# Kernel optimization log

Measured on AMD Instinct MI355X. Metric: run time of the kernel, lower is better.

## Reference

```python
import jax, jax.numpy as jnp
import numpy as np

B, H, W = 64, 224, 224
EPS = 1e-5


def setup_inputs() -> dict:
    key = jax.random.key(0)
    ks = jax.random.split(key, 8)
    n = lambda k, s, std: jax.random.normal(k, s, jnp.float32) * std
    return {
        "x": jax.random.normal(ks[0], (B, 1, H, W), jnp.float32),
        "conv1_w": n(ks[1], (24, 1, 3, 3), 0.2),
        "conv1_b": jnp.zeros((24,), jnp.float32),
        "bn1_g": jnp.ones((24,), jnp.float32),
        "bn1_b": jnp.zeros((24,), jnp.float32),
        "conv2_w": n(ks[2], (48, 24, 3, 3), 0.07),
        "conv2_b": jnp.zeros((48,), jnp.float32),
        "bn2_g": jnp.ones((48,), jnp.float32),
        "bn2_b": jnp.zeros((48,), jnp.float32),
        "fconv_w": n(ks[3], (48, 48, 56, 56), 0.003),
        "fconv_b": jnp.zeros((48,), jnp.float32),
        "lin1_w": n(ks[4], (24, 48), 0.02),
        "lin1_b": jnp.zeros((24,), jnp.float32),
        "lin2_w": n(ks[5], (4, 24), 0.01),
        "lin2_b": jnp.array([0.0, 0.0, 1.0, 0.0], jnp.float32),  # torch init: identity transform bias
    }


def conv2d(x, w, b):
    y = jax.lax.conv_general_dilated(x, w, (1, 1), ((1, 1), (1, 1)),
                                     dimension_numbers=("NCHW", "OIHW", "NCHW"))
    return y + b[None, :, None, None]


def batchnorm(x, g, b):
    # train-mode BN: batch statistics over (N, H, W), biased variance
    m = x.mean((0, 2, 3), keepdims=True)
    v = x.var((0, 2, 3), keepdims=True)
    return (x - m) * jax.lax.rsqrt(v + EPS) * g[None, :, None, None] + b[None, :, None, None]


def maxpool2(x):
    b, c, h, w = x.shape
    return x.reshape(b, c, h // 2, 2, w // 2, 2).max(axis=(3, 5))


def affine_grid(theta, h, w):
    # theta: [B,2,3]; align_corners=False normalized coords (torch default)
    xs = (jnp.arange(w, dtype=jnp.float32) * 2 + 1) / w - 1.0
    ys = (jnp.arange(h, dtype=jnp.float32) * 2 + 1) / h - 1.0
    gx, gy = jnp.meshgrid(xs, ys)                      # [H,W] each
    base = jnp.stack([gx, gy, jnp.ones_like(gx)], -1)  # [H,W,3] (x, y, 1)
    return jnp.einsum("bij,hwj->bhwi", theta, base)    # [B,H,W,2] -> (x, y)


def grid_sample(img, grid):
    # bilinear, zeros padding, align_corners=False (torch defaults)
    b, c, h, w = img.shape
    ix = ((grid[..., 0] + 1.0) * w - 1.0) * 0.5        # [B,H,W]
    iy = ((grid[..., 1] + 1.0) * h - 1.0) * 0.5
    x0 = jnp.floor(ix); y0 = jnp.floor(iy)
    x1 = x0 + 1.0; y1 = y0 + 1.0
    wx1 = ix - x0; wx0 = 1.0 - wx1
    wy1 = iy - y0; wy0 = 1.0 - wy1
    bidx = jnp.arange(b)[:, None, None]

    def tap(xf, yf, wgt):
        valid = (xf >= 0) & (xf < w) & (yf >= 0) & (yf < h)
        xi = jnp.clip(xf, 0, w - 1).astype(jnp.int32)
        yi = jnp.clip(yf, 0, h - 1).astype(jnp.int32)
        vals = img[bidx, :, yi, xi]                    # [B,H,W,C]
        return vals * (wgt * valid)[..., None]

    out = (tap(x0, y0, wx0 * wy0) + tap(x1, y0, wx1 * wy0)
           + tap(x0, y1, wx0 * wy1) + tap(x1, y1, wx1 * wy1))
    return jnp.transpose(out, (0, 3, 1, 2))            # [B,C,H,W]


def reference(x, conv1_w, conv1_b, bn1_g, bn1_b, conv2_w, conv2_b, bn2_g, bn2_b,
              fconv_w, fconv_b, lin1_w, lin1_b, lin2_w, lin2_b):
    b, _, h, w = x.shape
    x1 = maxpool2(jax.nn.relu(batchnorm(conv2d(x, conv1_w, conv1_b), bn1_g, bn1_b)))
    x1 = maxpool2(jax.nn.relu(batchnorm(conv2d(x1, conv2_w, conv2_b), bn2_g, bn2_b)))
    # final_conv with kernel 56 over a 56x56 map == full contraction
    feat = jnp.einsum("bchw,ochw->bo", x1, fconv_w) + fconv_b      # [B,48]
    theta4 = jax.nn.relu(feat @ lin1_w.T + lin1_b) @ lin2_w.T + lin2_b  # [B,4]
    tx, ty, scale, angle = theta4[:, 0], theta4[:, 1], theta4[:, 2], theta4[:, 3]
    c, s = jnp.cos(angle), jnp.sin(angle)
    # (T @ R @ S)[:, :2] built directly, fully vectorized over batch
    row0 = jnp.stack([scale * c, -scale * s, tx], -1)
    row1 = jnp.stack([scale * s, scale * c, ty], -1)
    theta = jnp.stack([row0, row1], 1)                 # [B,2,3]
    grid = affine_grid(theta, h, w)
    out = grid_sample(x, grid)
    return out, tx, ty, scale, angle
```

## Files before the change

### kernel.cpp

```cpp
#include <hip/hip_runtime.h>
#include <hip/hip_bf16.h>

#define NB 64
#define H0 224
#define W0 224
#define C1 24
#define C2 48
#define H1 112
#define W1 112
#define H2 56
#define W2 56
#define EPSV 1e-5f

#define WS_STATS1   0
#define WS_STATS2   432
#define WS_FEAT     1296
#define WS_B2       4368
#define WS_X2       11280
#define WS_FWT      (WS_X2 + 4818944)
#define WS_X1       9645072
#define WS_NEED_BIG ((size_t)(WS_X1 + 9633792) * 4)
#define OUT0_ELEMS  (NB*H0*W0)

typedef _Float16 v8h __attribute__((ext_vector_type(8)));
typedef float    v4f __attribute__((ext_vector_type(4)));

static __device__ __forceinline__ unsigned short f2h(float v) {
    _Float16 h = (_Float16)v;
    unsigned short us;
    __builtin_memcpy(&us, &h, 2);
    return us;
}

__global__ __launch_bounds__(256) void k_zero1(float* __restrict__ ws)
{
    int t = blockIdx.x * 256 + threadIdx.x;
    if (t < 432) ws[t] = 0.f;
}

__global__ __launch_bounds__(256) void k_stats_prep(
    const float* __restrict__ x, const float* __restrict__ w1, const float* __restrict__ b1,
    const float* __restrict__ w2, const float* __restrict__ fw,
    float* __restrict__ ws, _Float16* __restrict__ x1g, _Float16* __restrict__ fwt)
{
    __shared__ __align__(16) unsigned char smem[18432];
    const int tid = threadIdx.x;
    const int bid = blockIdx.x;

    if (bid >= 3136) {
        _Float16 (*T)[136] = (_Float16(*)[136])smem;
        const int p = bid - 3136;
        if (p < 54) {
            int t = p * 256 + tid;
            if (t >= 432 && t < WS_B2) ws[t] = 0.f;
            if (t < 13824) {
                int e = t & 7;
                int l = (t >> 3) & 63;
                int g = t >> 9;
                int q = l >> 4, ml = l & 15;
                int kp = g / 3, nt = g % 3;
                int ic = q * 8 + e;
                int oc = nt * 16 + ml;
                float v = (ic < C1) ? w2[(oc * C1 + ic) * 9 + kp] : 0.f;
                ((_Float16*)(ws + WS_B2))[t] = (_Float16)v;
            }
        }
        const int kb = p * 128;
#pragma unroll
        for (int t3 = 0; t3 < 6; t3++) {
            int li = tid + 256 * t3;
            int o = li >> 5, k4 = li & 31;
            float4 v = *(const float4*)&fw[(long)o * 150528 + kb + 4 * k4];
            T[o][4 * k4 + 0] = (_Float16)v.x;
            T[o][4 * k4 + 1] = (_Float16)v.y;
            T[o][4 * k4 + 2] = (_Float16)v.z;
            T[o][4 * k4 + 3] = (_Float16)v.w;
        }
        __syncthreads();
        uint4* dst = (uint4*)&fwt[(long)kb * 48];
#pragma unroll
        for (int t3 = 0; t3 < 3; t3++) {
            int u = tid + 256 * t3;
            int gg = u / 384;
            int rem = u % 384;
            int o = rem >> 3;
            int k8 = (rem & 7) * 8;
            dst[u] = *(const uint4*)&T[o][gg * 64 + k8];
        }
        return;
    }

    float (*xt)[36] = (float(*)[36])smem;
    unsigned int (*outt)[13] = (unsigned int(*)[13])(smem + 4896);
    float* sred = (float*)(smem + 18208);

    const int b = bid / 49;
    const int rem0 = bid % 49;
    const int py0 = (rem0 / 7) * 16, px0 = (rem0 % 7) * 16;
    const int iy0 = 2 * py0 - 1, ix0 = 2 * px0 - 1;
    const float* xb = x + b * (H0 * W0);

    for (int li = tid; li < 34 * 34; li += 256) {
        int ry = li / 34, rx = li % 34;
        int gy = iy0 + ry, gx = ix0 + rx;
        bool ok = (gy >= 0) & (gy < H0) & (gx >= 0) & (gx < W0);
        xt[ry][rx] = ok ? xb[gy * W0 + gx] : 0.f;
    }

    const int wid = tid >> 6;
    const int lane = tid & 63;
    const int c0 = wid * 6;

    const int c0s = __builtin_amdgcn_readfirstlane(c0);
    const float* __restrict__ wps = w1 + c0s * 9;
    float wr[54], br[6];
#pragma unroll
    for (int k = 0; k < 54; k++) wr[k] = wps[k];
#pragma unroll
    for (int c = 0; c < 6; c++) br[c] = b1[c0s + c];

    __syncthreads();

    float s[6] = {0.f, 0.f, 0.f, 0.f, 0.f, 0.f};
    float q[6] = {0.f, 0.f, 0.f, 0.f, 0.f, 0.f};
    const int pc = lane & 15;
    const int pr0 = lane >> 4;

#pragma unroll
    for (int pp = 0; pp < 4; pp++) {
        const int pr = pr0 + 4 * pp;
        float patch[16];
#pragma unroll
        for (int i2 = 0; i2 < 4; i2++)
#pragma unroll
            for (int j2 = 0; j2 < 4; j2++)
                patch[i2 * 4 + j2] = xt[2 * pr + i2][2 * pc + j2];

        unsigned int pk[3];
#pragma unroll
        for (int cp = 0; cp < 3; cp++) {
            unsigned int pv = 0;
#pragma unroll
            for (int h = 0; h < 2; h++) {
                int c = 2 * cp + h;
                float m4 = -1e30f;
#pragma unroll
                for (int sy = 0; sy < 2; sy++)
#pragma unroll
                    for (int sx = 0; sx < 2; sx++) {
                        float a = br[c];
#pragma unroll
                        for (int ky = 0; ky < 3; ky++)
#pragma unroll
                            for (int kx = 0; kx < 3; kx++)
                                a = fmaf(patch[(sy + ky) * 4 + (sx + kx)], wr[c * 9 + ky * 3 + kx], a);
                        s[c] += a;
                        q[c] = fmaf(a, a, q[c]);
                        m4 = fmaxf(m4, a);
                    }
                pv |= ((unsigned int)f2h(m4)) << (16 * h);
            }
            pk[cp] = pv;
        }
        int pos = pr * 16 + pc;
        outt[pos][wid * 3 + 0] = pk[0];
        outt[pos][wid * 3 + 1] = pk[1];
        outt[pos][wid * 3 + 2] = pk[2];
    }

#pragma unroll
    for (int c = 0; c < 6; c++) {
#pragma unroll
        for (int off = 32; off > 0; off >>= 1) {
            s[c] += __shfl_down(s[c], off, 64);
            q[c] += __shfl_down(q[c], off, 64);
        }
    }
    if (lane == 0) {
#pragma unroll
        for (int c = 0; c < 6; c++) {
            sred[c0 + c] = s[c];
            sred[C1 + c0 + c] = q[c];
        }
    }
    __syncthreads();

    if (tid < 2 * C1) {
        atomicAdd(&ws[WS_STATS1 + (bid & 7) * 2 * C1 + tid], sred[tid]);
    }

    for (int u = tid; u < 768; u += 256) {
        int pos = u / 3, prt = u % 3;
        int pr = pos >> 4, pcc = pos & 15;
        long p = (long)(b * H1 + (py0 + pr)) * W1 + (px0 + pcc);
        uint4 v;
        v.x = outt[pos][4 * prt + 0];
        v.y = outt[pos][4 * prt + 1];
        v.z = outt[pos][4 * prt + 2];
        v.w = outt[pos][4 * prt + 3];
        *(uint4*)(x1g + p * C1 + prt * 8) = v;
    }
}

__global__ __launch_bounds__(256, 2) void k_conv2_fused5(
    const _Float16* __restrict__ x1g, const _Float16* __restrict__ bpp,
    const float* __restrict__ g1, const float* __restrict__ bb1,
    const float* __restrict__ b2,
    float* __restrict__ ws, unsigned int* __restrict__ pooltu)
{
    __shared__ __align__(16) _Float16 x1t[2][10][18][32];
    __shared__ float alds[C1], bflds[C1];
    __shared__ float sred[2 * C2];

    const int tid = threadIdx.x;
    const int w = tid >> 6;
    const int lane = tid & 63;
    const int ml = lane & 15;
    const int qq = lane >> 4;

    v8h B[9][3];
#pragma unroll
    for (int kp = 0; kp < 9; kp++)
#pragma unroll
        for (int nt = 0; nt < 3; nt++)
            B[kp][nt] = *(const v8h*)&bpp[((kp * 3 + nt) * 64 + lane) * 8];

    if (tid < C1) {
        float s = 0.f, q = 0.f;
#pragma unroll
        for (int i = 0; i < 8; i++) {
            s += ws[WS_STATS1 + i * 2 * C1 + tid];
            q += ws[WS_STATS1 + i * 2 * C1 + C1 + tid];
        }
        const float N = (float)(NB * H0 * W0);
        float m = s / N;
        float v = q / N - m * m;
        float a = g1[tid] / sqrtf(v + EPSV);
        alds[tid] = a;
        bflds[tid] = bb1[tid] - m * a;
    }
    if (tid < 2 * C2) sred[tid] = 0.f;

    float bias[3] = {b2[ml], b2[16 + ml], b2[32 + ml]};

    int spart[3], spr[3], spc[3]; bool swrite[3];
#pragma unroll
    for (int it3 = 0; it3 < 3; it3++) {
        int li = tid + it3 * 256;
        swrite[it3] = li < 720;
        spart[it3] = li & 3;
        int pos = li >> 2;
        spr[it3] = pos / 18;
        spc[it3] = pos % 18;
    }

    const int nb = gridDim.x;
    const int NTILE = 6272;
    int qn = NTILE / nb, rn = NTILE % nb;
    int start = (blockIdx.x < rn) ? blockIdx.x * (qn + 1)
                                  : rn * (qn + 1) + (blockIdx.x - rn) * qn;
    int cnt = (blockIdx.x < rn) ? qn + 1 : qn;

    float svacc[3] = {0.f, 0.f, 0.f}, qvacc[3] = {0.f, 0.f, 0.f};

    v8h raw[3];
    bool inb_n[3];
    {
        int t = start;
        int tb = t / 98, rem = t % 98;
        int ty = (rem / 7) * 8, txx = (rem % 7) * 16;
#pragma unroll
        for (int it3 = 0; it3 < 3; it3++) {
#pragma unroll
            for (int e = 0; e < 8; e++) raw[it3][e] = (_Float16)0.f;
            int gy = ty - 1 + spr[it3], gx = txx - 1 + spc[it3];
            inb_n[it3] = swrite[it3] & (spart[it3] < 3) &
                         (gy >= 0) & (gy < H1) & (gx >= 0) & (gx < W1);
            if (inb_n[it3])
                raw[it3] = *(const v8h*)&x1g[((tb * H1 + gy) * W1 + gx) * C1 + spart[it3] * 8];
        }
    }
    __syncthreads();

#pragma unroll
    for (int it3 = 0; it3 < 3; it3++) {
        if (swrite[it3]) {
            v8h r8;
            if (inb_n[it3]) {
#pragma unroll
                for (int e = 0; e < 8; e++) {
                    int c = spart[it3] * 8 + e;
                    float vv = fmaxf(fmaf((float)raw[it3][e], alds[c], bflds[c]), 0.f);
                    r8[e] = (_Float16)vv;
                }
            } else {
#pragma unroll
                for (int e = 0; e < 8; e++) r8[e] = (_Float16)0.f;
            }
            *(v8h*)&x1t[0][spr[it3]][spc[it3]][spart[it3] * 8] = r8;
        }
    }
    __syncthreads();

    for (int it = 0; it < cnt; it++) {
        const int cur = it & 1;
        const int t = start + it;
        const int tb = t / 98, rem = t % 98;
        const int ty = (rem / 7) * 8, txx = (rem % 7) * 16;

        const bool haveNext = (it + 1 < cnt);
        if (haveNext) {
            int t2 = t + 1;
            int nb2 = t2 / 98, rem2 = t2 % 98;
            int ny = (rem2 / 7) * 8, nx = (rem2 % 7) * 16;
#pragma unroll
            for (int it3 = 0; it3 < 3; it3++) {
#pragma unroll
                for (int e = 0; e < 8; e++) raw[it3][e] = (_Float16)0.f;
                int gy = ny - 1 + spr[it3], gx = nx - 1 + spc[it3];
                inb_n[it3] = swrite[it3] & (spart[it3] < 3) &
                             (gy >= 0) & (gy < H1) & (gx >= 0) & (gx < W1);
                if (inb_n[it3])
                    raw[it3] = *(const v8h*)&x1g[((nb2 * H1 + gy) * W1 + gx) * C1 + spart[it3] * 8];
            }
        }

        v4f acc[2][3];
#pragma unroll
        for (int mt = 0; mt < 2; mt++)
#pragma unroll
            for (int nt = 0; nt < 3; nt++)
                acc[mt][nt] = (v4f){0.f, 0.f, 0.f, 0.f};

#pragma unroll
        for (int kp = 0; kp < 9; kp++) {
            const int ky = kp / 3, kx = kp % 3;
#pragma unroll
            for (int mt = 0; mt < 2; mt++) {
                const int r = 2 * w + mt;
                v8h a = *(const v8h*)&x1t[cur][r + ky][ml + kx][qq * 8];
                acc[mt][0] = __builtin_amdgcn_mfma_f32_16x16x32_f16(a, B[kp][0], acc[mt][0], 0, 0, 0);
                acc[mt][1] = __builtin_amdgcn_mfma_f32_16x16x32_f16(a, B[kp][1], acc[mt][1], 0, 0, 0);
                acc[mt][2] = __builtin_amdgcn_mfma_f32_16x16x32_f16(a, B[kp][2], acc[mt][2], 0, 0, 0);
            }
        }

#pragma unroll
        for (int nt = 0; nt < 3; nt++) {
            int oc = nt * 16 + ml;
            float z[2][4];
#pragma unroll
            for (int mt = 0; mt < 2; mt++)
#pragma unroll
                for (int rg = 0; rg < 4; rg++) {
                    float val = acc[mt][nt][rg] + bias[nt];
                    z[mt][rg] = val;
                    svacc[nt] += val;
                    qvacc[nt] = fmaf(val, val, qvacc[nt]);
                }
            int py = (ty >> 1) + w;
            float m0 = fmaxf(fmaxf(z[0][0], z[0][1]), fmaxf(z[1][0], z[1][1]));
            float m1 = fmaxf(fmaxf(z[0][2], z[0][3]), fmaxf(z[1][2], z[1][3]));
            int px0 = (txx >> 1) + qq * 2;
            int k = oc * 3136 + py * W2 + px0;
            unsigned int pk2 = (unsigned int)f2h(m0) | ((unsigned int)f2h(m1) << 16);
            pooltu[(((k >> 6) * NB + tb) << 5) + ((k & 63) >> 1)] = pk2;
        }

        if (haveNext) {
#pragma unroll
            for (int it3 = 0; it3 < 3; it3++) {
                if (swrite[it3]) {
                    v8h r8;
                    if (inb_n[it3]) {
#pragma unroll
                        for (int e = 0; e < 8; e++) {
                            int c = spart[it3] * 8 + e;
                            float vv = fmaxf(fmaf((float)raw[it3][e], alds[c], bflds[c]), 0.f);
                            r8[e] = (_Float16)vv;
                        }
                    } else {
#pragma unroll
                        for (int e = 0; e < 8; e++) r8[e] = (_Float16)0.f;
                    }
                    *(v8h*)&x1t[cur ^ 1][spr[it3]][spc[it3]][spart[it3] * 8] = r8;
                }
            }
        }
        __syncthreads();
    }

#pragma unroll
    for (int nt = 0; nt < 3; nt++) {
        float sv = svacc[nt], qv = qvacc[nt];
        sv += __shfl_xor(sv, 16, 64); qv += __shfl_xor(qv, 16, 64);
        sv += __shfl_xor(sv, 32, 64); qv += __shfl_xor(qv, 32, 64);
        if (qq == 0) {
            atomicAdd(&sred[nt * 16 + ml], sv);
            atomicAdd(&sred[C2 + nt * 16 + ml], qv);
        }
    }
    __syncthreads();
    if (tid < 2 * C2) {
        atomicAdd(&ws[WS_STATS2 + (blockIdx.x & 7) * 2 * C2 + tid], sred[tid]);
    }
}

__global__ __launch_bounds__(256) void k_fconv6(
    const unsigned int* __restrict__ pooltu, const _Float16* __restrict__ fwt,
    const float* __restrict__ ws, const float* __restrict__ g2, const float* __restrict__ bb2,
    float* __restrict__ feat)
{
    __shared__ __align__(16) _Float16 fwh[48][136];
    __shared__ __align__(16) _Float16 x2h[64][136];
    __shared__ float csh[2 * C2];

    const int tid = threadIdx.x;
    const int bx = blockIdx.x;

    const uint4* fsrc = (const uint4*)fwt + (long)bx * 768;
    const uint4* psrc = (const uint4*)pooltu + (long)bx * 1024;
    uint4 fr[3], pr[4];
#pragma unroll
    for (int t3 = 0; t3 < 3; t3++) fr[t3] = fsrc[tid + 256 * t3];
#pragma unroll
    for (int t4 = 0; t4 < 4; t4++) pr[t4] = psrc[tid + 256 * t4];

    if (tid < C2) {
        int c = tid;
        float s = 0.f, q = 0.f;
#pragma unroll
        for (int i = 0; i < 8; i++) {
            s += ws[WS_STATS2 + i * 2 * C2 + c];
            q += ws[WS_STATS2 + i * 2 * C2 + C2 + c];
        }
        const float N = (float)(NB * H1 * W1);
        float m = s / N;
        float v = q / N - m * m;
        float a = g2[c] / sqrtf(v + EPSV);
        csh[c] = a;
        csh[C2 + c] = bb2[c] - m * a;
    }
    __syncthreads();

#pragma unroll
    for (int t3 = 0; t3 < 3; t3++) {
        int li = tid + 256 * t3;
        int gg = li / 384;
        int o = (li % 384) / 8;
        int kin = (li & 7) * 8;
        *(uint4*)&fwh[o][gg * 64 + kin] = fr[t3];
    }
    const int c0 = (2 * bx) / 49, c1 = (2 * bx + 1) / 49;
    const float a0 = csh[c0], bf0 = csh[C2 + c0];
    const float a1 = csh[c1], bf1 = csh[C2 + c1];
#pragma unroll
    for (int t4 = 0; t4 < 4; t4++) {
        int li = tid + 256 * t4;
        int gg = li >> 9;
        int b = (li & 511) >> 3;
        int kin = (li & 7) * 8;
        float aa = gg ? a1 : a0;
        float bb = gg ? bf1 : bf0;
        union { uint4 u; v8h h; } cv;
        cv.u = pr[t4];
        v8h r8;
#pragma unroll
        for (int e = 0; e < 8; e++)
            r8[e] = (_Float16)fmaxf(fmaf((float)cv.h[e], aa, bb), 0.f);
        *(v8h*)&x2h[b][gg * 64 + kin] = r8;
    }
    __syncthreads();

    const int w = tid >> 6;
    const int lane = tid & 63;
    const int ml = lane & 15;
    const int qq = lane >> 4;

    v4f acc[3];
#pragma unroll
    for (int ot = 0; ot < 3; ot++) acc[ot] = (v4f){0.f, 0.f, 0.f, 0.f};

#pragma unroll
    for (int ks = 0; ks < 4; ks++) {
        v8h a = *(const v8h*)&x2h[w * 16 + ml][ks * 32 + qq * 8];
#pragma unroll
        for (int ot = 0; ot < 3; ot++) {
            v8h bb = *(const v8h*)&fwh[ot * 16 + ml][ks * 32 + qq * 8];
            acc[ot] = __builtin_amdgcn_mfma_f32_16x16x32_f16(a, bb, acc[ot], 0, 0, 0);
        }
    }

#pragma unroll
    for (int ot = 0; ot < 3; ot++)
#pragma unroll
        for (int rg = 0; rg < 4; rg++)
            atomicAdd(&feat[(w * 16 + qq * 4 + rg) * C2 + ot * 16 + ml], acc[ot][rg]);
}

__global__ __launch_bounds__(256) void k_sample4(
    const float* __restrict__ x, const float* __restrict__ feat, const float* __restrict__ fcb,
    const float* __restrict__ l1w, const float* __restrict__ l1b,
    const float* __restrict__ l2w, const float* __restrict__ l2b,
    float* __restrict__ out)
{
    __shared__ float hsh[24];
    __shared__ float th[4];
    const int b = blockIdx.y;
    const int tid = threadIdx.x;
    if (tid < 24) {
        float a = l1b[tid];
#pragma unroll
        for (int o = 0; o < C2; o++)
            a = fmaf(feat[b * C2 + o] + fcb[o], l1w[tid * C2 + o], a);
        hsh[tid] = fmaxf(a, 0.f);
    }
    __syncthreads();
    if (tid < 4) {
        float a = l2b[tid];
#pragma unroll
        for (int jj = 0; jj < 24; jj++) a = fmaf(hsh[jj], l2w[tid * 24 + jj], a);
        th[tid] = a;
        if (blockIdx.x == 0) out[OUT0_ELEMS + tid * NB + b] = a;
    }
    __syncthreads();

    const float tx = th[0], ty = th[1], sc = th[2], an = th[3];
    const float cc = cosf(an), ss = sinf(an);
    const float t00 = sc * cc, t01 = -sc * ss, t10 = sc * ss, t11 = sc * cc;
    const float* xb = x + b * (H0 * W0);

    int idx = (blockIdx.x * 256 + tid) * 2;
    int i = idx / W0, j = idx % W0;
    float ys = (2.f * (float)i + 1.f) / (float)H0 - 1.f;

    float o2[2];
#pragma unroll
    for (int px = 0; px < 2; px++) {
        float xs = (2.f * (float)(j + px) + 1.f) / (float)W0 - 1.f;
        float gx = t00 * xs + t01 * ys + tx;
        float gy = t10 * xs + t11 * ys + ty;
        float ix = ((gx + 1.f) * (float)W0 - 1.f) * 0.5f;
        float iy = ((gy + 1.f) * (float)H0 - 1.f) * 0.5f;
        float x0 = floorf(ix), y0 = floorf(iy);
        float x1f = x0 + 1.f, y1f = y0 + 1.f;
        float wx1 = ix - x0, wx0 = 1.f - wx1;
        float wy1 = iy - y0, wy0 = 1.f - wy1;
        auto tap = [&](float xf, float yf, float wgt) -> float {
            bool valid = (xf >= 0.f) & (xf < (float)W0) & (yf >= 0.f) & (yf < (float)H0);
            int xi = (int)fminf(fmaxf(xf, 0.f), (float)(W0 - 1));
            int yi = (int)fminf(fmaxf(yf, 0.f), (float)(H0 - 1));
            return valid ? xb[yi * W0 + xi] * wgt : 0.f;
        };
        o2[px] = tap(x0, y0, wx0 * wy0) + tap(x1f, y0, wx1 * wy0)
               + tap(x0, y1f, wx0 * wy1) + tap(x1f, y1f, wx1 * wy1);
    }
    *(float2*)&out[(b * H0 + i) * W0 + j] = make_float2(o2[0], o2[1]);
}

__global__ __launch_bounds__(256) void k_init(const float* __restrict__ w2, float* __restrict__ ws)
{
    int t = blockIdx.x * 256 + threadIdx.x;
    if (t < WS_B2) ws[t] = 0.f;
    if (t < 13824) {
        int e = t & 7;
        int l = (t >> 3) & 63;
        int g = t >> 9;
        int q = l >> 4, ml = l & 15;
        int kp = g / 3, nt = g % 3;
        int ic = q * 8 + e;
        int oc = nt * 16 + ml;
        float v = (ic < C1) ? w2[(oc * C1 + ic) * 9 + kp] : 0.f;
        ((_Float16*)(ws + WS_B2))[t] = (_Float16)v;
    }
}

__global__ __launch_bounds__(256) void k_conv1_stats(
    const float* __restrict__ x, const float* __restrict__ w1, const float* __restrict__ b1,
    float* __restrict__ ws)
{
    float s[C1], q[C1];
#pragma unroll
    for (int c = 0; c < C1; c++) { s[c] = 0.f; q[c] = 0.f; }
    const int NT = gridDim.x * 256;
    const int total = NB * H0 * W0;
    for (int p = blockIdx.x * 256 + threadIdx.x; p < total; p += NT) {
        int b = p / (H0 * W0);
        int r = p % (H0 * W0);
        int y = r / W0;
        int xx = r % W0;
        const float* xb = x + b * (H0 * W0);
        float patch[9];
#pragma unroll
        for (int dy = 0; dy < 3; dy++)
#pragma unroll
            for (int dx = 0; dx < 3; dx++) {
                int yy = y + dy - 1, xc = xx + dx - 1;
                bool ok = (yy >= 0) & (yy < H0) & (xc >= 0) & (xc < W0);
                patch[dy * 3 + dx] = ok ? xb[yy * W0 + xc] : 0.f;
            }
#pragma unroll
        for (int c = 0; c < C1; c++) {
            const float* wp = w1 + c * 9;
            float a = b1[c];
#pragma unroll
            for (int k = 0; k < 9; k++) a = fmaf(patch[k], wp[k], a);
            s[c] += a;
            q[c] = fmaf(a, a, q[c]);
        }
    }
#pragma unroll
    for (int c = 0; c < C1; c++) {
#pragma unroll
        for (int off = 32; off > 0; off >>= 1) {
            s[c] += __shfl_down(s[c], off, 64);
            q[c] += __shfl_down(q[c], off, 64);
        }
    }
    __shared__ float sred[2 * C1];
    if (threadIdx.x < 2 * C1) sred[threadIdx.x] = 0.f;
    __syncthreads();
    if ((threadIdx.x & 63) == 0) {
#pragma unroll
        for (int c = 0; c < C1; c++) {
            atomicAdd(&sred[c], s[c]);
            atomicAdd(&sred[C1 + c], q[c]);
        }
    }
    __syncthreads();
    if (threadIdx.x < 2 * C1) {
        atomicAdd(&ws[WS_STATS1 + (blockIdx.x & 7) * 2 * C1 + threadIdx.x], sred[threadIdx.x]);
    }
}

__global__ __launch_bounds__(256, 2) void k_conv2_fused(
    const float* __restrict__ x, const float* __restrict__ w1, const float* __restrict__ b1,
    const float* __restrict__ g1, const float* __restrict__ bb1,
    const _Float16* __restrict__ bpp, const float* __restrict__ b2,
    float* __restrict__ ws, float* __restrict__ pool)
{
    __shared__ float xt[22][38];
    __shared__ __align__(16) _Float16 x1t[10][18][32];
    __shared__ __align__(16) _Float16 Blds[13824];
    __shared__ float wlds[C1 * 9];
    __shared__ float blds[C1], alds[C1], bflds[C1];
    __shared__ float sred[2 * C2];

    const int tid = threadIdx.x;
    const int b = blockIdx.z;
    const int y0 = blockIdx.y * 8;
    const int x0 = blockIdx.x * 16;
    const float* xb = x + b * (H0 * W0);

    for (int li = tid; li < 13824 / 8; li += 256)
        ((uint4*)Blds)[li] = ((const uint4*)bpp)[li];

    if (tid < C1 * 9) wlds[tid] = w1[tid];
    if (tid < C1) {
        float s = 0.f, q = 0.f;
#pragma unroll
        for (int i = 0; i < 8; i++) {
            s += ws[WS_STATS1 + i * 2 * C1 + tid];
            q += ws[WS_STATS1 + i * 2 * C1 + C1 + tid];
        }
        const float N = (float)(NB * H0 * W0);
        float m = s / N;
        float v = q / N - m * m;
        float a = g1[tid] / sqrtf(v + EPSV);
        blds[tid] = b1[tid];
        alds[tid] = a;
        bflds[tid] = bb1[tid] - m * a;
    }
    if (tid < 2 * C2) sred[tid] = 0.f;

    const int oy0 = 2 * y0 - 3, ox0 = 2 * x0 - 3;
    for (int li = tid; li < 22 * 38; li += 256) {
        int ry = li / 38, rx = li % 38;
        int gy = oy0 + ry, gx = ox0 + rx;
        bool ok = (gy >= 0) & (gy < H0) & (gx >= 0) & (gx < W0);
        xt[ry][rx] = ok ? xb[gy * W0 + gx] : 0.f;
    }
    __syncthreads();

    if (tid < 180) {
        int pr = tid / 18, pc = tid % 18;
        int gy = y0 - 1 + pr, gx = x0 - 1 + pc;
        bool valid = (gy >= 0) & (gy < H1) & (gx >= 0) & (gx < W1);
        float patch[16];
#pragma unroll
        for (int dy = 0; dy < 4; dy++)
#pragma unroll
            for (int dx = 0; dx < 4; dx++)
                patch[dy * 4 + dx] = xt[2 * pr + dy][2 * pc + dx];
        unsigned int* dst = (unsigned int*)&x1t[pr][pc][0];
#pragma unroll
        for (int cp = 0; cp < 12; cp++) {
            unsigned int pk = 0;
#pragma unroll
            for (int h = 0; h < 2; h++) {
                int c = 2 * cp + h;
                float m4 = -1e30f;
#pragma unroll
                for (int py = 0; py < 2; py++)
#pragma unroll
                    for (int px = 0; px < 2; px++) {
                        float a = blds[c];
#pragma unroll
                        for (int ky = 0; ky < 3; ky++)
#pragma unroll
                            for (int kx = 0; kx < 3; kx++)
                                a = fmaf(patch[(py + ky) * 4 + (px + kx)], wlds[c * 9 + ky * 3 + kx], a);
                        m4 = fmaxf(m4, fmaf(a, alds[c], bflds[c]));
                    }
                float v = valid ? fmaxf(m4, 0.f) : 0.f;
                pk |= ((unsigned int)f2h(v)) << (16 * h);
            }
            dst[cp] = pk;
        }
        dst[12] = 0; dst[13] = 0; dst[14] = 0; dst[15] = 0;
    }
    __syncthreads();

    const int w = tid >> 6;
    const int lane = tid & 63;
    const int ml = lane & 15;
    const int q = lane >> 4;

    v4f acc[2][3];
#pragma unroll
    for (int mt = 0; mt < 2; mt++)
#pragma unroll
        for (int nt = 0; nt < 3; nt++)
            acc[mt][nt] = (v4f){0.f, 0.f, 0.f, 0.f};

#pragma unroll
    for (int kp = 0; kp < 9; kp++) {
        const int ky = kp / 3, kx = kp % 3;
        v8h B0 = *(const v8h*)&Blds[((kp * 3 + 0) * 64 + lane) * 8];
        v8h B1 = *(const v8h*)&Blds[((kp * 3 + 1) * 64 + lane) * 8];
        v8h B2 = *(const v8h*)&Blds[((kp * 3 + 2) * 64 + lane) * 8];
#pragma unroll
        for (int mt = 0; mt < 2; mt++) {
            const int r = 2 * w + mt;
            v8h a = *(const v8h*)&x1t[r + ky][ml + kx][q * 8];
            acc[mt][0] = __builtin_amdgcn_mfma_f32_16x16x32_f16(a, B0, acc[mt][0], 0, 0, 0);
            acc[mt][1] = __builtin_amdgcn_mfma_f32_16x16x32_f16(a, B1, acc[mt][1], 0, 0, 0);
            acc[mt][2] = __builtin_amdgcn_mfma_f32_16x16x32_f16(a, B2, acc[mt][2], 0, 0, 0);
        }
    }

#pragma unroll
    for (int nt = 0; nt < 3; nt++) {
        int oc = nt * 16 + ml;
        float bias = b2[oc];
        float z[2][4];
        float sv = 0.f, qv = 0.f;
#pragma unroll
        for (int mt = 0; mt < 2; mt++)
#pragma unroll
            for (int rg = 0; rg < 4; rg++) {
                float val = acc[mt][nt][rg] + bias;
                z[mt][rg] = val;
                sv += val;
                qv = fmaf(val, val, qv);
            }
        sv += __shfl_xor(sv, 16, 64); qv += __shfl_xor(qv, 16, 64);
        sv += __shfl_xor(sv, 32, 64); qv += __shfl_xor(qv, 32, 64);
        if (q == 0) { atomicAdd(&sred[oc], sv); atomicAdd(&sred[C2 + oc], qv); }

        int py = (y0 >> 1) + w;
#pragma unroll
        for (int j = 0; j < 2; j++) {
            float m = fmaxf(fmaxf(z[0][2 * j], z[0][2 * j + 1]),
                            fmaxf(z[1][2 * j], z[1][2 * j + 1]));
            int px = (x0 >> 1) + q * 2 + j;
            pool[((b * C2 + oc) * H2 + py) * W2 + px] = m;
        }
    }
    __syncthreads();
    if (tid < 2 * C2) {
        int cp = (blockIdx.x + 7 * blockIdx.y + 31 * blockIdx.z) & 7;
        atomicAdd(&ws[WS_STATS2 + cp * 2 * C2 + tid], sred[tid]);
    }
}

#define KC 512
#define KSUB 128
__global__ __launch_bounds__(256) void k_fconv(
    const float* __restrict__ pool, const float* __restrict__ ws,
    const float* __restrict__ g2, const float* __restrict__ bb2,
    const float* __restrict__ fw, float* __restrict__ feat)
{
    __shared__ float fwt[C2][KSUB + 1];
    __shared__ float x2t[NB][KSUB + 1];
    __shared__ float csh[2 * C2];
    if (threadIdx.x < C2) {
        int c = threadIdx.x;
        float s = 0.f, q = 0.f;
#pragma unroll
        for (int i = 0; i < 8; i++) {
            s += ws[WS_STATS2 + i * 2 * C2 + c];
            q += ws[WS_STATS2 + i * 2 * C2 + C2 + c];
        }
        const float N = (float)(NB * H1 * W1);
        float m = s / N;
        float v = q / N - m * m;
        float a = g2[c] / sqrtf(v + EPSV);
        csh[c] = a;
        csh[C2 + c] = bb2[c] - m * a;
    }
    int k0 = blockIdx.x * KC;
    int i = threadIdx.x / 16, j = threadIdx.x % 16;
    float acc[3][4] = {{0.f}};
    for (int sub = 0; sub < KC / KSUB; sub++) {
        int kb = k0 + sub * KSUB;
        __syncthreads();
        for (int li = threadIdx.x; li < C2 * KSUB; li += 256) {
            int o = li / KSUB, k = li % KSUB;
            fwt[o][k] = fw[o * 150528 + kb + k];
        }
        for (int li = threadIdx.x; li < NB * KSUB; li += 256) {
            int b = li / KSUB, k = li % KSUB;
            int kk = kb + k;
            int c = kk / (H2 * W2);
            float v = pool[b * 150528 + kk];
            x2t[b][k] = fmaxf(fmaf(v, csh[c], csh[C2 + c]), 0.f);
        }
        __syncthreads();
        for (int k = 0; k < KSUB; k++) {
            float fa[3], xv[4];
#pragma unroll
            for (int c = 0; c < 3; c++) fa[c] = fwt[i + 16 * c][k];
#pragma unroll
            for (int d = 0; d < 4; d++) xv[d] = x2t[j + 16 * d][k];
#pragma unroll
            for (int c = 0; c < 3; c++)
#pragma unroll
                for (int d = 0; d < 4; d++)
                    acc[c][d] = fmaf(fa[c], xv[d], acc[c][d]);
        }
    }
#pragma unroll
    for (int c = 0; c < 3; c++)
#pragma unroll
        for (int d = 0; d < 4; d++)
            atomicAdd(&feat[(j + 16 * d) * C2 + (i + 16 * c)], acc[c][d]);
}

__global__ __launch_bounds__(256) void k_sample(
    const float* __restrict__ x, const float* __restrict__ feat, const float* __restrict__ fcb,
    const float* __restrict__ l1w, const float* __restrict__ l1b,
    const float* __restrict__ l2w, const float* __restrict__ l2b,
    float* __restrict__ out)
{
    __shared__ float hsh[24];
    __shared__ float th[4];
    int b = blockIdx.y;
    int tid = threadIdx.x;
    if (tid < 24) {
        float a = l1b[tid];
        for (int o = 0; o < C2; o++)
            a = fmaf(feat[b * C2 + o] + fcb[o], l1w[tid * C2 + o], a);
        hsh[tid] = fmaxf(a, 0.f);
    }
    __syncthreads();
    if (tid < 4) {
        float a = l2b[tid];
        for (int jj = 0; jj < 24; jj++) a = fmaf(hsh[jj], l2w[tid * 24 + jj], a);
        th[tid] = a;
        if (blockIdx.x == 0) out[OUT0_ELEMS + tid * NB + b] = a;
    }
    __syncthreads();

    int idx = blockIdx.x * 256 + tid;
    int i = idx / W0, j = idx % W0;
    float tx = th[0], ty = th[1], sc = th[2], an = th[3];
    float cc = cosf(an), ss = sinf(an);
    float t00 = sc * cc, t01 = -sc * ss, t10 = sc * ss, t11 = sc * cc;
    float xs = (2.f * (float)j + 1.f) / (float)W0 - 1.f;
    float ys = (2.f * (float)i + 1.f) / (float)H0 - 1.f;
    float gx = t00 * xs + t01 * ys + tx;
    float gy = t10 * xs + t11 * ys + ty;
    float ix = ((gx + 1.f) * (float)W0 - 1.f) * 0.5f;
    float iy = ((gy + 1.f) * (float)H0 - 1.f) * 0.5f;
    float x0 = floorf(ix), y0 = floorf(iy);
    float x1f = x0 + 1.f, y1f = y0 + 1.f;
    float wx1 = ix - x0, wx0 = 1.f - wx1;
    float wy1 = iy - y0, wy0 = 1.f - wy1;
    const float* xb = x + b * (H0 * W0);
    auto tap = [&](float xf, float yf, float wgt) -> float {
        bool valid = (xf >= 0.f) & (xf < (float)W0) & (yf >= 0.f) & (yf < (float)H0);
        int xi = (int)fminf(fmaxf(xf, 0.f), (float)(W0 - 1));
        int yi = (int)fminf(fmaxf(yf, 0.f), (float)(H0 - 1));
        return valid ? xb[yi * W0 + xi] * wgt : 0.f;
    };
    float o = tap(x0, y0, wx0 * wy0) + tap(x1f, y0, wx1 * wy0)
            + tap(x0, y1f, wx0 * wy1) + tap(x1f, y1f, wx1 * wy1);
    out[(b * H0 + i) * W0 + j] = o;
}

extern "C" void kernel_launch(void* const* d_in, const int* in_sizes, int n_in,
                              void* d_out, int out_size, void* d_ws, size_t ws_size,
                              hipStream_t stream)
{
    const float* x    = (const float*)d_in[0];
    const float* c1w  = (const float*)d_in[1];
    const float* c1b  = (const float*)d_in[2];
    const float* bn1g = (const float*)d_in[3];
    const float* bn1b = (const float*)d_in[4];
    const float* c2w  = (const float*)d_in[5];
    const float* c2b  = (const float*)d_in[6];
    const float* bn2g = (const float*)d_in[7];
    const float* bn2b = (const float*)d_in[8];
    const float* fw   = (const float*)d_in[9];
    const float* fcb  = (const float*)d_in[10];
    const float* l1w  = (const float*)d_in[11];
    const float* l1b  = (const float*)d_in[12];
    const float* l2w  = (const float*)d_in[13];
    const float* l2b  = (const float*)d_in[14];
    float* ws  = (float*)d_ws;
    float* out = (float*)d_out;

    if (ws_size >= WS_NEED_BIG) {
        k_zero1<<<dim3(2), 256, 0, stream>>>(ws);
        k_stats_prep<<<dim3(4312), 256, 0, stream>>>(
            x, c1w, c1b, c2w, fw, ws, (_Float16*)(ws + WS_X1), (_Float16*)(ws + WS_FWT));
        k_conv2_fused5<<<dim3(512), 256, 0, stream>>>(
            (const _Float16*)(ws + WS_X1), (const _Float16*)(ws + WS_B2),
            bn1g, bn1b, c2b, ws, (unsigned int*)(ws + WS_X2));
        k_fconv6<<<dim3(1176), 256, 0, stream>>>(
            (const unsigned int*)(ws + WS_X2), (const _Float16*)(ws + WS_FWT),
            ws, bn2g, bn2b, ws + WS_FEAT);
        k_sample4<<<dim3(98, 64), 256, 0, stream>>>(
            x, ws + WS_FEAT, fcb, l1w, l1b, l2w, l2b, out);
    } else {
        k_init<<<dim3(54), 256, 0, stream>>>(c2w, ws);
        k_conv1_stats<<<dim3(1024), 256, 0, stream>>>(x, c1w, c1b, ws);
        k_conv2_fused<<<dim3(7, 14, 64), 256, 0, stream>>>(
            x, c1w, c1b, bn1g, bn1b, (const _Float16*)(ws + WS_B2), c2b, ws, ws + WS_X2);
        k_fconv<<<dim3(150528 / KC), 256, 0, stream>>>(ws + WS_X2, ws, bn2g, bn2b, fw, ws + WS_FEAT);
        k_sample<<<dim3(196, 64), 256, 0, stream>>>(x, ws + WS_FEAT, fcb, l1w, l1b, l2w, l2b, out);
    }
}
```

Measured before the change: 220.0 us.

## Enlarge conv2 spatial tile to 16x16 with 4 M-tiles per wave

The conv2 fused kernel now processes 16x16 output tiles instead of 8x16, so each wave computes four row M-tiles and writes two pooled rows per tile. This halves the tile count and shrinks the relative halo overhead on the shared-memory staging loads. Staging now fills only the 24 real channels with a 3-way split, and the padding slots are zeroed once up front. The cost is doubled LDS and more accumulator registers, which may lower occupancy under the 2-blocks-per-SM launch bound. The tiny zeroing kernel is also replaced by hipMemsetAsync.

```diff
diff --git a/kernel.cpp b/kernel.cpp
--- a/kernel.cpp
+++ b/kernel.cpp
@@ -30,12 +30,6 @@
     unsigned short us;
     __builtin_memcpy(&us, &h, 2);
     return us;
-}
-
-__global__ __launch_bounds__(256) void k_zero1(float* __restrict__ ws)
-{
-    int t = blockIdx.x * 256 + threadIdx.x;
-    if (t < 432) ws[t] = 0.f;
 }
 
 __global__ __launch_bounds__(256) void k_stats_prep(
@@ -202,13 +196,13 @@
     }
 }
 
-__global__ __launch_bounds__(256, 2) void k_conv2_fused5(
+__global__ __launch_bounds__(256, 2) void k_conv2_fused6(
     const _Float16* __restrict__ x1g, const _Float16* __restrict__ bpp,
     const float* __restrict__ g1, const float* __restrict__ bb1,
     const float* __restrict__ b2,
     float* __restrict__ ws, unsigned int* __restrict__ pooltu)
 {
-    __shared__ __align__(16) _Float16 x1t[2][10][18][32];
+    __shared__ __align__(16) _Float16 x1t[2][18][18][32];
     __shared__ float alds[C1], bflds[C1];
     __shared__ float sred[2 * C2];
 
@@ -241,21 +235,32 @@
     }
     if (tid < 2 * C2) sred[tid] = 0.f;
 
+    {
+        v8h z8;
+#pragma unroll
+        for (int e = 0; e < 8; e++) z8[e] = (_Float16)0.f;
+        for (int li = tid; li < 2 * 18 * 18; li += 256) {
+            int bu = li / 324, pos = li % 324;
+            *(v8h*)&x1t[bu][pos / 18][pos % 18][24] = z8;
+        }
+    }
+
     float bias[3] = {b2[ml], b2[16 + ml], b2[32 + ml]};
 
-    int spart[3], spr[3], spc[3]; bool swrite[3];
-#pragma unroll
-    for (int it3 = 0; it3 < 3; it3++) {
-        int li = tid + it3 * 256;
-        swrite[it3] = li < 720;
-        spart[it3] = li & 3;
-        int pos = li >> 2;
-        spr[it3] = pos / 18;
-        spc[it3] = pos % 18;
+    int spart[4], spr[4], spc[4]; bool sv[4];
+#pragma unroll
+    for (int s4 = 0; s4 < 4; s4++) {
+        int li = tid + s4 * 256;
+        sv[s4] = li < 972;
+        int part = li % 3;
+        int pos = li / 3;
+        spart[s4] = part;
+        spr[s4] = pos / 18;
+        spc[s4] = pos % 18;
     }
 
     const int nb = gridDim.x;
-    const int NTILE = 6272;
+    const int NTILE = 3136;
     int qn = NTILE / nb, rn = NTILE % nb;
     int start = (blockIdx.x < rn) ? blockIdx.x * (qn + 1)
                                   : rn * (qn + 1) + (blockIdx.x - rn) * qn;
@@ -263,41 +268,40 @@
 
     float svacc[3] = {0.f, 0.f, 0.f}, qvacc[3] = {0.f, 0.f, 0.f};
 
-    v8h raw[3];
-    bool inb_n[3];
+    v8h raw[4];
+    bool inb_n[4];
     {
         int t = start;
-        int tb = t / 98, rem = t % 98;
-        int ty = (rem / 7) * 8, txx = (rem % 7) * 16;
-#pragma unroll
-        for (int it3 = 0; it3 < 3; it3++) {
-#pragma unroll
-            for (int e = 0; e < 8; e++) raw[it3][e] = (_Float16)0.f;
-            int gy = ty - 1 + spr[it3], gx = txx - 1 + spc[it3];
-            inb_n[it3] = swrite[it3] & (spart[it3] < 3) &
-                         (gy >= 0) & (gy < H1) & (gx >= 0) & (gx < W1);
-            if (inb_n[it3])
-                raw[it3] = *(const v8h*)&x1g[((tb * H1 + gy) * W1 + gx) * C1 + spart[it3] * 8];
-        }
-    }
-    __syncthreads();
-
-#pragma unroll
-    for (int it3 = 0; it3 < 3; it3++) {
-        if (swrite[it3]) {
+        int tb = t / 49, rem = t % 49;
+        int ty = (rem / 7) * 16, txx = (rem % 7) * 16;
+#pragma unroll
+        for (int s4 = 0; s4 < 4; s4++) {
+#pragma unroll
+            for (int e = 0; e < 8; e++) raw[s4][e] = (_Float16)0.f;
+            int gy = ty - 1 + spr[s4], gx = txx - 1 + spc[s4];
+            inb_n[s4] = sv[s4] & (gy >= 0) & (gy < H1) & (gx >= 0) & (gx < W1);
+            if (inb_n[s4])
+                raw[s4] = *(const v8h*)&x1g[((tb * H1 + gy) * W1 + gx) * C1 + spart[s4] * 8];
+        }
+    }
+    __syncthreads();
+
+#pragma unroll
+    for (int s4 = 0; s4 < 4; s4++) {
+        if (sv[s4]) {
             v8h r8;
-            if (inb_n[it3]) {
+            if (inb_n[s4]) {
 #pragma unroll
                 for (int e = 0; e < 8; e++) {
-                    int c = spart[it3] * 8 + e;
-                    float vv = fmaxf(fmaf((float)raw[it3][e], alds[c], bflds[c]), 0.f);
+                    int c = spart[s4] * 8 + e;
+                    float vv = fmaxf(fmaf((float)raw[s4][e], alds[c], bflds[c]), 0.f);
                     r8[e] = (_Float16)vv;
                 }
             } else {
 #pragma unroll
                 for (int e = 0; e < 8; e++) r8[e] = (_Float16)0.f;
             }
-            *(v8h*)&x1t[0][spr[it3]][spc[it3]][spart[it3] * 8] = r8;
+            *(v8h*)&x1t[0][spr[s4]][spc[s4]][spart[s4] * 8] = r8;
         }
     }
     __syncthreads();
@@ -305,29 +309,28 @@
     for (int it = 0; it < cnt; it++) {
         const int cur = it & 1;
         const int t = start + it;
-        const int tb = t / 98, rem = t % 98;
-        const int ty = (rem / 7) * 8, txx = (rem % 7) * 16;
+        const int tb = t / 49, rem = t % 49;
+        const int ty = (rem / 7) * 16, txx = (rem % 7) * 16;
 
         const bool haveNext = (it + 1 < cnt);
         if (haveNext) {
             int t2 = t + 1;
-            int nb2 = t2 / 98, rem2 = t2 % 98;
-            int ny = (rem2 / 7) * 8, nx = (rem2 % 7) * 16;
-#pragma unroll
-            for (int it3 = 0; it3 < 3; it3++) {
-#pragma unroll
-                for (int e = 0; e < 8; e++) raw[it3][e] = (_Float16)0.f;
-                int gy = ny - 1 + spr[it3], gx = nx - 1 + spc[it3];
-                inb_n[it3] = swrite[it3] & (spart[it3] < 3) &
-                             (gy >= 0) & (gy < H1) & (gx >= 0) & (gx < W1);
-                if (inb_n[it3])
-                    raw[it3] = *(const v8h*)&x1g[((nb2 * H1 + gy) * W1 + gx) * C1 + spart[it3] * 8];
+            int nb2 = t2 / 49, rem2 = t2 % 49;
+            int ny = (rem2 / 7) * 16, nx = (rem2 % 7) * 16;
+#pragma unroll
+            for (int s4 = 0; s4 < 4; s4++) {
+#pragma unroll
+                for (int e = 0; e < 8; e++) raw[s4][e] = (_Float16)0.f;
+                int gy = ny - 1 + spr[s4], gx = nx - 1 + spc[s4];
+                inb_n[s4] = sv[s4] & (gy >= 0) & (gy < H1) & (gx >= 0) & (gx < W1);
+                if (inb_n[s4])
+                    raw[s4] = *(const v8h*)&x1g[((nb2 * H1 + gy) * W1 + gx) * C1 + spart[s4] * 8];
             }
         }
 
-        v4f acc[2][3];
-#pragma unroll
-        for (int mt = 0; mt < 2; mt++)
+        v4f acc[4][3];
+#pragma unroll
+        for (int mt = 0; mt < 4; mt++)
 #pragma unroll
             for (int nt = 0; nt < 3; nt++)
                 acc[mt][nt] = (v4f){0.f, 0.f, 0.f, 0.f};
@@ -336,8 +339,8 @@
         for (int kp = 0; kp < 9; kp++) {
             const int ky = kp / 3, kx = kp % 3;
 #pragma unroll
-            for (int mt = 0; mt < 2; mt++) {
-                const int r = 2 * w + mt;
+            for (int mt = 0; mt < 4; mt++) {
+                const int r = 4 * w + mt;
                 v8h a = *(const v8h*)&x1t[cur][r + ky][ml + kx][qq * 8];
                 acc[mt][0] = __builtin_amdgcn_mfma_f32_16x16x32_f16(a, B[kp][0], acc[mt][0], 0, 0, 0);
                 acc[mt][1] = __builtin_amdgcn_mfma_f32_16x16x32_f16(a, B[kp][1], acc[mt][1], 0, 0, 0);
@@ -348,9 +351,9 @@
 #pragma unroll
         for (int nt = 0; nt < 3; nt++) {
             int oc = nt * 16 + ml;
-            float z[2][4];
-#pragma unroll
-            for (int mt = 0; mt < 2; mt++)
+            float z[4][4];
+#pragma unroll
+            for (int mt = 0; mt < 4; mt++)
 #pragma unroll
                 for (int rg = 0; rg < 4; rg++) {
                     float val = acc[mt][nt][rg] + bias[nt];
@@ -358,32 +361,37 @@
                     svacc[nt] += val;
                     qvacc[nt] = fmaf(val, val, qvacc[nt]);
                 }
-            int py = (ty >> 1) + w;
-            float m0 = fmaxf(fmaxf(z[0][0], z[0][1]), fmaxf(z[1][0], z[1][1]));
-            float m1 = fmaxf(fmaxf(z[0][2], z[0][3]), fmaxf(z[1][2], z[1][3]));
-            int px0 = (txx >> 1) + qq * 2;
-            int k = oc * 3136 + py * W2 + px0;
-            unsigned int pk2 = (unsigned int)f2h(m0) | ((unsigned int)f2h(m1) << 16);
-            pooltu[(((k >> 6) * NB + tb) << 5) + ((k & 63) >> 1)] = pk2;
+#pragma unroll
+            for (int h = 0; h < 2; h++) {
+                int py = (ty >> 1) + 2 * w + h;
+                float m0 = fmaxf(fmaxf(z[2 * h][0], z[2 * h][1]),
+                                 fmaxf(z[2 * h + 1][0], z[2 * h + 1][1]));
+                float m1 = fmaxf(fmaxf(z[2 * h][2], z[2 * h][3]),
+                                 fmaxf(z[2 * h + 1][2], z[2 * h + 1][3]));
+                int px0 = (txx >> 1) + qq * 2;
+                int k = oc * 3136 + py * W2 + px0;
+                unsigned int pk2 = (unsigned int)f2h(m0) | ((unsigned int)f2h(m1) << 16);
+                pooltu[(((k >> 6) * NB + tb) << 5) + ((k & 63) >> 1)] = pk2;
+            }
         }
 
         if (haveNext) {
 #pragma unroll
-            for (int it3 = 0; it3 < 3; it3++) {
-                if (swrite[it3]) {
+            for (int s4 = 0; s4 < 4; s4++) {
+                if (sv[s4]) {
                     v8h r8;
-                    if (inb_n[it3]) {
+                    if (inb_n[s4]) {
 #pragma unroll
                         for (int e = 0; e < 8; e++) {
-                            int c = spart[it3] * 8 + e;
-                            float vv = fmaxf(fmaf((float)raw[it3][e], alds[c], bflds[c]), 0.f);
+                            int c = spart[s4] * 8 + e;
+                            float vv = fmaxf(fmaf((float)raw[s4][e], alds[c], bflds[c]), 0.f);
                             r8[e] = (_Float16)vv;
                         }
                     } else {
 #pragma unroll
                         for (int e = 0; e < 8; e++) r8[e] = (_Float16)0.f;
                     }
-                    *(v8h*)&x1t[cur ^ 1][spr[it3]][spc[it3]][spart[it3] * 8] = r8;
+                    *(v8h*)&x1t[cur ^ 1][spr[s4]][spc[s4]][spart[s4] * 8] = r8;
                 }
             }
         }
@@ -392,11 +400,11 @@
 
 #pragma unroll
     for (int nt = 0; nt < 3; nt++) {
-        float sv = svacc[nt], qv = qvacc[nt];
-        sv += __shfl_xor(sv, 16, 64); qv += __shfl_xor(qv, 16, 64);
-        sv += __shfl_xor(sv, 32, 64); qv += __shfl_xor(qv, 32, 64);
+        float sv2 = svacc[nt], qv = qvacc[nt];
+        sv2 += __shfl_xor(sv2, 16, 64); qv += __shfl_xor(qv, 16, 64);
+        sv2 += __shfl_xor(sv2, 32, 64); qv += __shfl_xor(qv, 32, 64);
         if (qq == 0) {
-            atomicAdd(&sred[nt * 16 + ml], sv);
+            atomicAdd(&sred[nt * 16 + ml], sv2);
             atomicAdd(&sred[C2 + nt * 16 + ml], qv);
         }
     }
@@ -922,10 +930,10 @@
     float* out = (float*)d_out;
 
     if (ws_size >= WS_NEED_BIG) {
-        k_zero1<<<dim3(2), 256, 0, stream>>>(ws);
+        hipMemsetAsync(ws, 0, 432 * sizeof(float), stream);
         k_stats_prep<<<dim3(4312), 256, 0, stream>>>(
             x, c1w, c1b, c2w, fw, ws, (_Float16*)(ws + WS_X1), (_Float16*)(ws + WS_FWT));
-        k_conv2_fused5<<<dim3(512), 256, 0, stream>>>(
+        k_conv2_fused6<<<dim3(512), 256, 0, stream>>>(
             (const _Float16*)(ws + WS_X1), (const _Float16*)(ws + WS_B2),
             bn1g, bn1b, c2b, ws, (unsigned int*)(ws + WS_X2));
         k_fconv6<<<dim3(1176), 256, 0, stream>>>(
```

New measurement: 218.9 us, median of 2. No clear change (-0.5%).
